# Kernel tuning notes

Hardware: AMD Instinct MI355X
Metric: run time of the kernel (lower is better)

The kernel has to match this reference:

```python
import jax, jax.numpy as jnp
import numpy as np

V, E, H = 32000, 512, 512
EH = 2 * H  # encoder output size (bidirectional)
B, T, S = 32, 64, 128


def setup_inputs() -> dict:
    key = jax.random.key(0)
    ks = jax.random.split(key, 16)
    s = 0.02
    return {
        "tgt_inputs": jax.random.randint(ks[0], (B, T), 0, V),
        "hidden": jax.random.normal(ks[1], (2, B, H), jnp.float32),
        "encoder_outputs": jax.random.normal(ks[2], (B, S, EH), jnp.float32),
        "src_mask": jnp.ones((B, S), jnp.bool_),
        "embedding": jax.random.normal(ks[3], (V, E), jnp.float32) * s,
        "Wa": jax.random.normal(ks[4], (EH, H), jnp.float32) * s,  # Linear(H -> 2H), weight [out,in]
        "w_ih0": jax.random.normal(ks[5], (3 * H, E + EH), jnp.float32) * s,
        "w_hh0": jax.random.normal(ks[6], (3 * H, H), jnp.float32) * s,
        "b_ih0": jax.random.normal(ks[7], (3 * H,), jnp.float32) * s,
        "b_hh0": jax.random.normal(ks[8], (3 * H,), jnp.float32) * s,
        "w_ih1": jax.random.normal(ks[9], (3 * H, H), jnp.float32) * s,
        "w_hh1": jax.random.normal(ks[10], (3 * H, H), jnp.float32) * s,
        "b_ih1": jax.random.normal(ks[11], (3 * H,), jnp.float32) * s,
        "b_hh1": jax.random.normal(ks[12], (3 * H,), jnp.float32) * s,
        "fc_w": jax.random.normal(ks[13], (V, H + EH), jnp.float32) * s,
        "fc_b": jax.random.normal(ks[14], (V,), jnp.float32) * s,
    }


def _gru_cell(x, h, w_ih, w_hh, b_ih, b_hh):
    # PyTorch GRU cell math
    gi = x @ w_ih.T + b_ih
    gh = h @ w_hh.T + b_hh
    i_r, i_z, i_n = jnp.split(gi, 3, axis=-1)
    h_r, h_z, h_n = jnp.split(gh, 3, axis=-1)
    r = jax.nn.sigmoid(i_r + h_r)
    z = jax.nn.sigmoid(i_z + h_z)
    n = jnp.tanh(i_n + r * h_n)
    return (1.0 - z) * n + z * h


def reference(tgt_inputs, hidden, encoder_outputs, src_mask, embedding, Wa,
              w_ih0, w_hh0, b_ih0, b_hh0, w_ih1, w_hh1, b_ih1, b_hh1,
              fc_w, fc_b):
    scale = 1.0 / jnp.sqrt(jnp.asarray(EH, encoder_outputs.dtype))

    def step(h, tok):
        emb = embedding[tok]                                   # [B,E]
        q = h[-1] @ Wa.T                                       # [B,2H] general attention
        scores = jnp.einsum('be,bse->bs', q, encoder_outputs) * scale
        scores = jnp.where(src_mask, scores, -jnp.inf)
        attn = jax.nn.softmax(scores, axis=-1)                 # [B,S]
        ctx = jnp.einsum('bs,bse->be', attn, encoder_outputs)  # [B,2H]
        x0 = jnp.concatenate([emb, ctx], axis=-1)              # [B,E+2H]
        h0 = _gru_cell(x0, h[0], w_ih0, w_hh0, b_ih0, b_hh0)
        h1 = _gru_cell(h0, h[1], w_ih1, w_hh1, b_ih1, b_hh1)
        logits = jnp.concatenate([h1, ctx], axis=-1) @ fc_w.T + fc_b  # [B,V]
        return jnp.stack([h0, h1]), logits

    # decode steps consume tokens 0..T-2 (teacher forcing)
    toks = tgt_inputs[:, :-1].T                                # [T-1,B]
    _, logits = jax.lax.scan(step, hidden, toks)
    return jnp.transpose(logits, (1, 0, 2))                    # [B,T-1,V]
```

## Files before the change

### kernel.cpp

```cpp
#include <hip/hip_runtime.h>
#include <cstdint>

typedef __attribute__((ext_vector_type(8))) short bf16x8;
typedef __attribute__((ext_vector_type(4))) float f32x4;
typedef __attribute__((ext_vector_type(2))) int i32x2;

__device__ __forceinline__ float bf2f(unsigned short u) {
  union { unsigned int i; float f; } v;
  v.i = ((unsigned int)u) << 16;
  return v.f;
}
__device__ __forceinline__ unsigned short f2bf(float f) {
  union { float f; unsigned int i; } v;
  v.f = f;
  unsigned int x = v.i;
  return (unsigned short)((x + 0x7FFFu + ((x >> 16) & 1u)) >> 16);
}

__device__ __forceinline__ void st_f32_coh(float* p, float v) {
  asm volatile("global_store_dword %0, %1, off sc0 sc1" :: "v"(p), "v"(v) : "memory");
}
__device__ __forceinline__ void st_u16_coh(unsigned short* p, unsigned int v) {
  asm volatile("global_store_short %0, %1, off sc0 sc1" :: "v"(p), "v"(v) : "memory");
}
__device__ __forceinline__ void st_b64_coh(void* p, i32x2 v) {
  asm volatile("global_store_dwordx2 %0, %1, off sc0 sc1" :: "v"(p), "v"(v) : "memory");
}

struct StepParams {
  const int* tgt;
  const int* mask;
  const float* embedding;
  const float* enc;
  const float* Wa;
  const float* hidden;
  const float* w_ih0; const float* w_hh0; const float* b_ih0; const float* b_hh0;
  const float* w_ih1; const float* w_hh1; const float* b_ih1; const float* b_hh1;
  float* h0buf;
  float* h1buf;
  float* x0b;
  unsigned short* encb;
  unsigned short* encwt;
  unsigned short* states;
  unsigned int* bars;
};

__device__ __forceinline__ void gbar(unsigned int* c) {
  asm volatile("s_waitcnt vmcnt(0)" ::: "memory");
  __syncthreads();
  if (threadIdx.x == 0) {
    __hip_atomic_fetch_add(c, 1u, __ATOMIC_RELAXED, __HIP_MEMORY_SCOPE_AGENT);
    while (__hip_atomic_load(c, __ATOMIC_RELAXED, __HIP_MEMORY_SCOPE_AGENT) < 256u)
      __builtin_amdgcn_s_sleep(1);
  }
  __syncthreads();
}

__device__ __forceinline__ void stage(const float* __restrict__ src, int ldk,
                                      int t0, int tid, float* __restrict__ xsh) {
#pragma unroll
  for (int u = 0; u < 32; u++)
    xsh[u * 257 + tid] = src[(size_t)u * ldk + t0 + tid];
}

__device__ __forceinline__ void gru_phase(
    const float* __restrict__ x, int xK,
    const float* __restrict__ hprev,
    const float* __restrict__ w_ih, const float* __restrict__ w_hh,
    const float* __restrict__ b_ih, const float* __restrict__ b_hh,
    float* __restrict__ hout, unsigned short* states, int srow,
    int w, int tid, float* xsh, float* red) {
  int b = tid & 31;
  int jl = (tid >> 5) & 1;
  int kq = tid >> 6;
  int j = w * 2 + jl;
  int kb = kq * 64;
  float gr = 0.f, gz = 0.f, gin = 0.f, ghn = 0.f;
  for (int t0 = 0; t0 < xK; t0 += 256) {
    __syncthreads();
    stage(x, xK, t0, tid, xsh);
    __syncthreads();
    const float4* w0p = (const float4*)(w_ih + (size_t)j * xK + t0 + kb);
    const float4* w1p = (const float4*)(w_ih + (size_t)(j + 512) * xK + t0 + kb);
    const float4* w2p = (const float4*)(w_ih + (size_t)(j + 1024) * xK + t0 + kb);
    const float* xr = xsh + b * 257 + kb;
#pragma unroll 4
    for (int k4 = 0; k4 < 16; k4++) {
      float4 wa = w0p[k4], wb = w1p[k4], wc = w2p[k4];
      float xv0 = xr[k4 * 4 + 0], xv1 = xr[k4 * 4 + 1];
      float xv2 = xr[k4 * 4 + 2], xv3 = xr[k4 * 4 + 3];
      gr = fmaf(wa.x, xv0, gr); gr = fmaf(wa.y, xv1, gr);
      gr = fmaf(wa.z, xv2, gr); gr = fmaf(wa.w, xv3, gr);
      gz = fmaf(wb.x, xv0, gz); gz = fmaf(wb.y, xv1, gz);
      gz = fmaf(wb.z, xv2, gz); gz = fmaf(wb.w, xv3, gz);
      gin = fmaf(wc.x, xv0, gin); gin = fmaf(wc.y, xv1, gin);
      gin = fmaf(wc.z, xv2, gin); gin = fmaf(wc.w, xv3, gin);
    }
  }
  for (int t0 = 0; t0 < 512; t0 += 256) {
    __syncthreads();
    stage(hprev, 512, t0, tid, xsh);
    __syncthreads();
    const float4* w0p = (const float4*)(w_hh + (size_t)j * 512 + t0 + kb);
    const float4* w1p = (const float4*)(w_hh + (size_t)(j + 512) * 512 + t0 + kb);
    const float4* w2p = (const float4*)(w_hh + (size_t)(j + 1024) * 512 + t0 + kb);
    const float* xr = xsh + b * 257 + kb;
#pragma unroll 4
    for (int k4 = 0; k4 < 16; k4++) {
      float4 wa = w0p[k4], wb = w1p[k4], wc = w2p[k4];
      float xv0 = xr[k4 * 4 + 0], xv1 = xr[k4 * 4 + 1];
      float xv2 = xr[k4 * 4 + 2], xv3 = xr[k4 * 4 + 3];
      gr = fmaf(wa.x, xv0, gr); gr = fmaf(wa.y, xv1, gr);
      gr = fmaf(wa.z, xv2, gr); gr = fmaf(wa.w, xv3, gr);
      gz = fmaf(wb.x, xv0, gz); gz = fmaf(wb.y, xv1, gz);
      gz = fmaf(wb.z, xv2, gz); gz = fmaf(wb.w, xv3, gz);
      ghn = fmaf(wc.x, xv0, ghn); ghn = fmaf(wc.y, xv1, ghn);
      ghn = fmaf(wc.z, xv2, ghn); ghn = fmaf(wc.w, xv3, ghn);
    }
  }
  red[tid * 4 + 0] = gr;
  red[tid * 4 + 1] = gz;
  red[tid * 4 + 2] = gin;
  red[tid * 4 + 3] = ghn;
  __syncthreads();
  if (tid < 64) {
#pragma unroll
    for (int g = 1; g < 4; g++) {
      gr += red[(tid + g * 64) * 4 + 0];
      gz += red[(tid + g * 64) * 4 + 1];
      gin += red[(tid + g * 64) * 4 + 2];
      ghn += red[(tid + g * 64) * 4 + 3];
    }
    gr += b_ih[j] + b_hh[j];
    gz += b_ih[j + 512] + b_hh[j + 512];
    gin += b_ih[j + 1024];
    ghn += b_hh[j + 1024];
    float r = 1.f / (1.f + __expf(-gr));
    float zz = 1.f / (1.f + __expf(-gz));
    float nv = gin + r * ghn;
    float e2 = __expf(-2.f * fabsf(nv));
    float th = (1.f - e2) / (1.f + e2);
    th = copysignf(th, nv);
    float hp = hprev[b * 512 + j];
    float hn = (1.f - zz) * th + zz * hp;
    st_f32_coh(hout + b * 512 + j, hn);
    if (states) states[(size_t)(srow + b) * 1536 + j] = f2bf(hn);
  }
}

__global__ __launch_bounds__(256, 1) void k_steps(StepParams p) {
  __shared__ float xsh[32 * 257];
  __shared__ float red[1024];
  __shared__ float h1sh[512];
  __shared__ float ssh[128];
  __shared__ float red2[128];
  int tid = threadIdx.x;
  int w = blockIdx.x;

  {
    int idx = w * 256 + tid;
    if (idx < 16384) st_f32_coh(p.h0buf + idx, p.hidden[idx]);
    else if (idx < 32768) st_f32_coh(p.h1buf + (idx - 16384), p.hidden[idx]);
    for (int r = 0; r < 16; r++) {
      size_t i4 = (size_t)r * 65536 + idx;
      float4 v = *(const float4*)(p.enc + i4 * 4);
      ushort4 o;
      o.x = f2bf(v.x); o.y = f2bf(v.y); o.z = f2bf(v.z); o.w = f2bf(v.w);
      union { ushort4 u; i32x2 d; } cv;
      cv.u = o;
      st_b64_coh(p.encb + i4 * 4, cv.d);
    }
    for (int blk = w; blk < 512; blk += 256) {
      int b = blk >> 4, s0 = (blk & 15) * 8;
      __syncthreads();
      for (int u = 0; u < 32; u++) {
        int f = u * 256 + tid;
        xsh[f] = p.enc[((size_t)b * 128 + s0 + (f >> 10)) * 1024 + (f & 1023)];
      }
      __syncthreads();
      float acc0[8] = {}, acc1[8] = {};
      for (int e = 0; e < 1024; e++) {
        float w0 = p.Wa[e * 512 + tid];
        float w1 = p.Wa[e * 512 + tid + 256];
#pragma unroll
        for (int si = 0; si < 8; si++) {
          float ev = xsh[si * 1024 + e];
          acc0[si] += w0 * ev;
          acc1[si] += w1 * ev;
        }
      }
#pragma unroll
      for (int si = 0; si < 8; si++) {
        st_u16_coh(p.encwt + ((size_t)b * 128 + s0 + si) * 512 + tid, f2bf(acc0[si]));
        st_u16_coh(p.encwt + ((size_t)b * 128 + s0 + si) * 512 + tid + 256, f2bf(acc1[si]));
      }
    }
  }
  unsigned int* bar = p.bars;
  gbar(bar++);

  int xcd = w & 7, loc = w >> 3;
  int ab = xcd * 4 + (loc >> 3);
  int ec = loc & 7;
  for (int t = 0; t < 63; t++) {
    const float* h1prev = p.h1buf + (size_t)t * 16384;
    float* x0t = p.x0b + (size_t)t * 49152;
    {
      float2 hv = *(const float2*)(h1prev + ab * 512 + tid * 2);
      h1sh[tid * 2] = hv.x;
      h1sh[tid * 2 + 1] = hv.y;
    }
    __syncthreads();
    {
      int s = tid & 127, part = tid >> 7;
      const unsigned short* ew = p.encwt + ((size_t)ab * 128 + s) * 512 + part * 256;
      const float* hh = h1sh + part * 256;
      float pacc = 0.f;
#pragma unroll 8
      for (int hc = 0; hc < 32; hc++) {
        bf16x8 v = *(const bf16x8*)(ew + hc * 8);
        const float* h8 = hh + hc * 8;
        pacc += bf2f((unsigned short)v[0]) * h8[0] + bf2f((unsigned short)v[1]) * h8[1]
              + bf2f((unsigned short)v[2]) * h8[2] + bf2f((unsigned short)v[3]) * h8[3]
              + bf2f((unsigned short)v[4]) * h8[4] + bf2f((unsigned short)v[5]) * h8[5]
              + bf2f((unsigned short)v[6]) * h8[6] + bf2f((unsigned short)v[7]) * h8[7];
      }
      red[tid] = pacc;
    }
    __syncthreads();
    if (tid < 128) {
      float sc = (red[tid] + red[tid + 128]) * 0.03125f;
      if (p.mask[ab * 128 + tid] == 0) sc = -__builtin_huge_valf();
      ssh[tid] = sc;
      red2[tid] = sc;
    }
    __syncthreads();
    for (int st = 64; st > 0; st >>= 1) {
      if (tid < st) red2[tid] = fmaxf(red2[tid], red2[tid + st]);
      __syncthreads();
    }
    float mx = red2[0];
    __syncthreads();
    if (tid < 128) {
      float e = __expf(ssh[tid] - mx);
      ssh[tid] = e;
      red2[tid] = e;
    }
    __syncthreads();
    for (int st = 64; st > 0; st >>= 1) {
      if (tid < st) red2[tid] += red2[tid + st];
      __syncthreads();
    }
    float inv = 1.f / red2[0];
    __syncthreads();
    if (tid < 128) ssh[tid] *= inv;
    __syncthreads();
    {
      int el = tid & 127, sh_ = tid >> 7;
      const unsigned short* eb = p.encb + (size_t)ab * 131072 + ec * 128 + el;
      int sbase = sh_ * 64;
      float c = 0.f;
#pragma unroll 8
      for (int s2 = 0; s2 < 64; s2++)
        c += ssh[sbase + s2] * bf2f(eb[(size_t)(sbase + s2) * 1024]);
      red[tid] = c;
    }
    __syncthreads();
    if (tid < 128) {
      float cv = red[tid] + red[tid + 128];
      st_f32_coh(x0t + ab * 1536 + 512 + ec * 128 + tid, cv);
      p.states[(size_t)(t * 32 + ab) * 1536 + 512 + ec * 128 + tid] = f2bf(cv);
    }
    {
      int tok = p.tgt[ab * 64 + t];
      if (tid < 64)
        st_f32_coh(x0t + ab * 1536 + ec * 64 + tid,
                   p.embedding[(size_t)tok * 512 + ec * 64 + tid]);
    }
    gbar(bar++);
    gru_phase(x0t, 1536, p.h0buf + (size_t)t * 16384, p.w_ih0, p.w_hh0, p.b_ih0,
              p.b_hh0, p.h0buf + (size_t)(t + 1) * 16384,
              (unsigned short*)nullptr, 0, w, tid, xsh, red);
    gbar(bar++);
    gru_phase(p.h0buf + (size_t)(t + 1) * 16384, 512, p.h1buf + (size_t)t * 16384,
              p.w_ih1, p.w_hh1, p.b_ih1, p.b_hh1,
              p.h1buf + (size_t)(t + 1) * 16384, p.states, t * 32, w, tid, xsh, red);
    gbar(bar++);
  }
}

__global__ __launch_bounds__(256) void k_cvt_fcw(const float* __restrict__ w,
                                                 unsigned short* __restrict__ o) {
  size_t i = ((size_t)blockIdx.x * 256 + threadIdx.x) * 8;
  float4 a = *(const float4*)(w + i);
  float4 b = *(const float4*)(w + i + 4);
  ushort4 lo, hi;
  lo.x = f2bf(a.x); lo.y = f2bf(a.y); lo.z = f2bf(a.z); lo.w = f2bf(a.w);
  hi.x = f2bf(b.x); hi.y = f2bf(b.y); hi.z = f2bf(b.z); hi.w = f2bf(b.w);
  *(ushort4*)(o + i) = lo;
  *(ushort4*)(o + i + 4) = hi;
}

template <bool PRE>
__global__ __launch_bounds__(256) void k_gemm(
    const unsigned short* __restrict__ states,
    const float* __restrict__ fc_w,
    const unsigned short* __restrict__ fcwb,
    const float* __restrict__ fc_b,
    float* __restrict__ out) {
  __shared__ unsigned short Ash[128 * 40];
  __shared__ unsigned short Bsh[128 * 40];
  int tid = threadIdx.x;
  int bx = blockIdx.x;
  int bid = (bx & 7) * 500 + (bx >> 3);
  int m0 = (bid & 15) * 128;
  int n0 = (bid >> 4) * 128;
  int lane = tid & 63, wave = tid >> 6;
  int q = lane >> 4, l16 = lane & 15;
  int wrow = (wave >> 1) * 64, wcol = (wave & 1) * 64;
  int arow = tid >> 1, ahalf = tid & 1;
  f32x4 acc[4][4] = {};
  const unsigned short* ag = states + (size_t)(m0 + arow) * 1536 + ahalf * 16;
  const float* bg = fc_w + (size_t)(n0 + arow) * 1536 + ahalf * 16;
  const unsigned short* bgb = PRE ? fcwb + (size_t)(n0 + arow) * 1536 + ahalf * 16 : nullptr;
  for (int k0 = 0; k0 < 1536; k0 += 32) {
    {
      const int4* src = (const int4*)(ag + k0);
      int4* dst = (int4*)(Ash + arow * 40 + ahalf * 16);
      dst[0] = src[0];
      dst[1] = src[1];
    }
    if constexpr (PRE) {
      const int4* src = (const int4*)(bgb + k0);
      int4* dst = (int4*)(Bsh + arow * 40 + ahalf * 16);
      dst[0] = src[0];
      dst[1] = src[1];
    } else {
      const float4* src = (const float4*)(bg + k0);
      __align__(16) unsigned short us[16];
#pragma unroll
      for (int i = 0; i < 4; i++) {
        float4 v = src[i];
        us[i * 4 + 0] = f2bf(v.x);
        us[i * 4 + 1] = f2bf(v.y);
        us[i * 4 + 2] = f2bf(v.z);
        us[i * 4 + 3] = f2bf(v.w);
      }
      int4* dst = (int4*)(Bsh + arow * 40 + ahalf * 16);
      dst[0] = ((int4*)us)[0];
      dst[1] = ((int4*)us)[1];
    }
    __syncthreads();
    bf16x8 av[4], bv[4];
#pragma unroll
    for (int i = 0; i < 4; i++) {
      av[i] = *(const bf16x8*)(Ash + (wrow + i * 16 + l16) * 40 + q * 8);
      bv[i] = *(const bf16x8*)(Bsh + (wcol + i * 16 + l16) * 40 + q * 8);
    }
#pragma unroll
    for (int mi = 0; mi < 4; mi++)
#pragma unroll
      for (int ni = 0; ni < 4; ni++)
        acc[mi][ni] = __builtin_amdgcn_mfma_f32_16x16x32_bf16(av[mi], bv[ni], acc[mi][ni], 0, 0, 0);
    __syncthreads();
  }
  float fb[4];
#pragma unroll
  for (int ni = 0; ni < 4; ni++) fb[ni] = fc_b[n0 + wcol + ni * 16 + l16];
#pragma unroll
  for (int mi = 0; mi < 4; mi++) {
#pragma unroll
    for (int r = 0; r < 4; r++) {
      int grow = m0 + wrow + mi * 16 + q * 4 + r;
      if (grow < 2016) {
        int tt = grow >> 5, bb = grow & 31;
        float* op = out + (size_t)bb * 2016000 + (size_t)tt * 32000 + n0 + wcol;
#pragma unroll
        for (int ni = 0; ni < 4; ni++)
          op[ni * 16 + l16] = acc[mi][ni][r] + fb[ni];
      }
    }
  }
}

extern "C" void kernel_launch(void* const* d_in, const int* in_sizes, int n_in,
                              void* d_out, int out_size, void* d_ws, size_t ws_size,
                              hipStream_t stream) {
  const int* tgt = (const int*)d_in[0];
  const float* hidden = (const float*)d_in[1];
  const float* enc = (const float*)d_in[2];
  const int* mask = (const int*)d_in[3];
  const float* embedding = (const float*)d_in[4];
  const float* Wa = (const float*)d_in[5];
  const float* w_ih0 = (const float*)d_in[6];
  const float* w_hh0 = (const float*)d_in[7];
  const float* b_ih0 = (const float*)d_in[8];
  const float* b_hh0 = (const float*)d_in[9];
  const float* w_ih1 = (const float*)d_in[10];
  const float* w_hh1 = (const float*)d_in[11];
  const float* b_ih1 = (const float*)d_in[12];
  const float* b_hh1 = (const float*)d_in[13];
  const float* fc_w = (const float*)d_in[14];
  const float* fc_b = (const float*)d_in[15];
  float* out = (float*)d_out;
  char* ws = (char*)d_ws;

  float* h0buf = (float*)(ws + 0);
  float* h1buf = (float*)(ws + 4194304);
  float* x0b = (float*)(ws + 8388608);
  unsigned short* encb = (unsigned short*)(ws + 20774912);
  unsigned short* encwt = (unsigned short*)(ws + 29163520);
  unsigned short* states = (unsigned short*)(ws + 33357824);
  unsigned int* bars = (unsigned int*)(ws + 39649280);
  const size_t FCWB_OFF = 41943040ull;
  unsigned short* fcwb = (unsigned short*)(ws + FCWB_OFF);
  bool pre = ws_size >= FCWB_OFF + 98304000ull;

  hipMemsetAsync(bars, 0, 4096, stream);
  if (pre) k_cvt_fcw<<<24000, 256, 0, stream>>>(fc_w, fcwb);

  StepParams p;
  p.tgt = tgt; p.mask = mask; p.embedding = embedding; p.enc = enc; p.Wa = Wa;
  p.hidden = hidden;
  p.w_ih0 = w_ih0; p.w_hh0 = w_hh0; p.b_ih0 = b_ih0; p.b_hh0 = b_hh0;
  p.w_ih1 = w_ih1; p.w_hh1 = w_hh1; p.b_ih1 = b_ih1; p.b_hh1 = b_hh1;
  p.h0buf = h0buf; p.h1buf = h1buf; p.x0b = x0b;
  p.encb = encb; p.encwt = encwt; p.states = states; p.bars = bars;

  k_steps<<<dim3(256), dim3(256), 0, stream>>>(p);

  if (pre) k_gemm<true><<<4000, 256, 0, stream>>>(states, fc_w, fcwb, fc_b, out);
  else k_gemm<false><<<4000, 256, 0, stream>>>(states, fc_w, nullptr, fc_b, out);
}
```

Baseline: 5.196 ms.

## Double threads per block in persistent decode kernel, splitting K reductions finer

Raises the persistent step kernel from 256 to 512 threads per block and re-partitions every phase (encoder preprocessing, attention scores, context, GRU matvecs) so each thread covers half the reduction range, with wider cross-thread reductions. The goal is more in-flight memory requests and latency hiding per CU in the latency-bound recurrent loop. The trade-off is extra shared-memory reduction work and larger __syncthreads costs. Some code paths may be inconsistent, for example the global barrier still counts 256 blocks and the GRU reduction now relies on red sized 2048.

```diff
diff --git a/kernel.cpp b/kernel.cpp
--- a/kernel.cpp
+++ b/kernel.cpp
@@ -56,13 +56,6 @@
   __syncthreads();
 }
 
-__device__ __forceinline__ void stage(const float* __restrict__ src, int ldk,
-                                      int t0, int tid, float* __restrict__ xsh) {
-#pragma unroll
-  for (int u = 0; u < 32; u++)
-    xsh[u * 257 + tid] = src[(size_t)u * ldk + t0 + tid];
-}
-
 __device__ __forceinline__ void gru_phase(
     const float* __restrict__ x, int xK,
     const float* __restrict__ hprev,
@@ -74,18 +67,23 @@
   int jl = (tid >> 5) & 1;
   int kq = tid >> 6;
   int j = w * 2 + jl;
-  int kb = kq * 64;
+  int kb = kq * 32;
   float gr = 0.f, gz = 0.f, gin = 0.f, ghn = 0.f;
   for (int t0 = 0; t0 < xK; t0 += 256) {
     __syncthreads();
-    stage(x, xK, t0, tid, xsh);
+#pragma unroll
+    for (int u = 0; u < 16; u++) {
+      int idx = u * 512 + tid;
+      xsh[(idx >> 8) * 257 + (idx & 255)] =
+          x[(size_t)(idx >> 8) * xK + t0 + (idx & 255)];
+    }
     __syncthreads();
     const float4* w0p = (const float4*)(w_ih + (size_t)j * xK + t0 + kb);
     const float4* w1p = (const float4*)(w_ih + (size_t)(j + 512) * xK + t0 + kb);
     const float4* w2p = (const float4*)(w_ih + (size_t)(j + 1024) * xK + t0 + kb);
     const float* xr = xsh + b * 257 + kb;
-#pragma unroll 4
-    for (int k4 = 0; k4 < 16; k4++) {
+#pragma unroll
+    for (int k4 = 0; k4 < 8; k4++) {
       float4 wa = w0p[k4], wb = w1p[k4], wc = w2p[k4];
       float xv0 = xr[k4 * 4 + 0], xv1 = xr[k4 * 4 + 1];
       float xv2 = xr[k4 * 4 + 2], xv3 = xr[k4 * 4 + 3];
@@ -99,14 +97,19 @@
   }
   for (int t0 = 0; t0 < 512; t0 += 256) {
     __syncthreads();
-    stage(hprev, 512, t0, tid, xsh);
+#pragma unroll
+    for (int u = 0; u < 16; u++) {
+      int idx = u * 512 + tid;
+      xsh[(idx >> 8) * 257 + (idx & 255)] =
+          hprev[(size_t)(idx >> 8) * 512 + t0 + (idx & 255)];
+    }
     __syncthreads();
     const float4* w0p = (const float4*)(w_hh + (size_t)j * 512 + t0 + kb);
     const float4* w1p = (const float4*)(w_hh + (size_t)(j + 512) * 512 + t0 + kb);
     const float4* w2p = (const float4*)(w_hh + (size_t)(j + 1024) * 512 + t0 + kb);
     const float* xr = xsh + b * 257 + kb;
-#pragma unroll 4
-    for (int k4 = 0; k4 < 16; k4++) {
+#pragma unroll
+    for (int k4 = 0; k4 < 8; k4++) {
       float4 wa = w0p[k4], wb = w1p[k4], wc = w2p[k4];
       float xv0 = xr[k4 * 4 + 0], xv1 = xr[k4 * 4 + 1];
       float xv2 = xr[k4 * 4 + 2], xv3 = xr[k4 * 4 + 3];
@@ -125,7 +128,7 @@
   __syncthreads();
   if (tid < 64) {
 #pragma unroll
-    for (int g = 1; g < 4; g++) {
+    for (int g = 1; g < 8; g++) {
       gr += red[(tid + g * 64) * 4 + 0];
       gz += red[(tid + g * 64) * 4 + 1];
       gin += red[(tid + g * 64) * 4 + 2];
@@ -148,9 +151,9 @@
   }
 }
 
-__global__ __launch_bounds__(256, 1) void k_steps(StepParams p) {
+__global__ __launch_bounds__(512, 4) void k_steps(StepParams p) {
   __shared__ float xsh[32 * 257];
-  __shared__ float red[1024];
+  __shared__ float red[2048];
   __shared__ float h1sh[512];
   __shared__ float ssh[128];
   __shared__ float red2[128];
@@ -158,11 +161,12 @@
   int w = blockIdx.x;
 
   {
-    int idx = w * 256 + tid;
+    int idx = w * 512 + tid;
     if (idx < 16384) st_f32_coh(p.h0buf + idx, p.hidden[idx]);
     else if (idx < 32768) st_f32_coh(p.h1buf + (idx - 16384), p.hidden[idx]);
-    for (int r = 0; r < 16; r++) {
-      size_t i4 = (size_t)r * 65536 + idx;
+#pragma unroll
+    for (int r = 0; r < 8; r++) {
+      size_t i4 = (size_t)r * 131072 + idx;
       float4 v = *(const float4*)(p.enc + i4 * 4);
       ushort4 o;
       o.x = f2bf(v.x); o.y = f2bf(v.y); o.z = f2bf(v.z); o.w = f2bf(v.w);
@@ -173,27 +177,21 @@
     for (int blk = w; blk < 512; blk += 256) {
       int b = blk >> 4, s0 = (blk & 15) * 8;
       __syncthreads();
-      for (int u = 0; u < 32; u++) {
-        int f = u * 256 + tid;
+#pragma unroll
+      for (int u = 0; u < 16; u++) {
+        int f = u * 512 + tid;
         xsh[f] = p.enc[((size_t)b * 128 + s0 + (f >> 10)) * 1024 + (f & 1023)];
       }
       __syncthreads();
-      float acc0[8] = {}, acc1[8] = {};
+      float acc[8] = {};
       for (int e = 0; e < 1024; e++) {
         float w0 = p.Wa[e * 512 + tid];
-        float w1 = p.Wa[e * 512 + tid + 256];
-#pragma unroll
-        for (int si = 0; si < 8; si++) {
-          float ev = xsh[si * 1024 + e];
-          acc0[si] += w0 * ev;
-          acc1[si] += w1 * ev;
-        }
+#pragma unroll
+        for (int si = 0; si < 8; si++) acc[si] += w0 * xsh[si * 1024 + e];
       }
 #pragma unroll
-      for (int si = 0; si < 8; si++) {
-        st_u16_coh(p.encwt + ((size_t)b * 128 + s0 + si) * 512 + tid, f2bf(acc0[si]));
-        st_u16_coh(p.encwt + ((size_t)b * 128 + s0 + si) * 512 + tid + 256, f2bf(acc1[si]));
-      }
+      for (int si = 0; si < 8; si++)
+        st_u16_coh(p.encwt + ((size_t)b * 128 + s0 + si) * 512 + tid, f2bf(acc[si]));
     }
   }
   unsigned int* bar = p.bars;
@@ -205,19 +203,15 @@
   for (int t = 0; t < 63; t++) {
     const float* h1prev = p.h1buf + (size_t)t * 16384;
     float* x0t = p.x0b + (size_t)t * 49152;
-    {
-      float2 hv = *(const float2*)(h1prev + ab * 512 + tid * 2);
-      h1sh[tid * 2] = hv.x;
-      h1sh[tid * 2 + 1] = hv.y;
-    }
+    h1sh[tid] = h1prev[ab * 512 + tid];
     __syncthreads();
     {
       int s = tid & 127, part = tid >> 7;
-      const unsigned short* ew = p.encwt + ((size_t)ab * 128 + s) * 512 + part * 256;
-      const float* hh = h1sh + part * 256;
+      const unsigned short* ew = p.encwt + ((size_t)ab * 128 + s) * 512 + part * 128;
+      const float* hh = h1sh + part * 128;
       float pacc = 0.f;
-#pragma unroll 8
-      for (int hc = 0; hc < 32; hc++) {
+#pragma unroll
+      for (int hc = 0; hc < 16; hc++) {
         bf16x8 v = *(const bf16x8*)(ew + hc * 8);
         const float* h8 = hh + hc * 8;
         pacc += bf2f((unsigned short)v[0]) * h8[0] + bf2f((unsigned short)v[1]) * h8[1]
@@ -229,7 +223,8 @@
     }
     __syncthreads();
     if (tid < 128) {
-      float sc = (red[tid] + red[tid + 128]) * 0.03125f;
+      float sc = red[tid] + red[tid + 128] + red[tid + 256] + red[tid + 384];
+      sc *= 0.03125f;
       if (p.mask[ab * 128 + tid] == 0) sc = -__builtin_huge_valf();
       ssh[tid] = sc;
       red2[tid] = sc;
@@ -258,16 +253,16 @@
     {
       int el = tid & 127, sh_ = tid >> 7;
       const unsigned short* eb = p.encb + (size_t)ab * 131072 + ec * 128 + el;
-      int sbase = sh_ * 64;
+      int sbase = sh_ * 32;
       float c = 0.f;
 #pragma unroll 8
-      for (int s2 = 0; s2 < 64; s2++)
+      for (int s2 = 0; s2 < 32; s2++)
         c += ssh[sbase + s2] * bf2f(eb[(size_t)(sbase + s2) * 1024]);
       red[tid] = c;
     }
     __syncthreads();
     if (tid < 128) {
-      float cv = red[tid] + red[tid + 128];
+      float cv = red[tid] + red[tid + 128] + red[tid + 256] + red[tid + 384];
       st_f32_coh(x0t + ab * 1536 + 512 + ec * 128 + tid, cv);
       p.states[(size_t)(t * 32 + ab) * 1536 + 512 + ec * 128 + tid] = f2bf(cv);
     }
@@ -427,7 +422,7 @@
   p.h0buf = h0buf; p.h1buf = h1buf; p.x0b = x0b;
   p.encb = encb; p.encwt = encwt; p.states = states; p.bars = bars;
 
-  k_steps<<<dim3(256), dim3(256), 0, stream>>>(p);
+  k_steps<<<dim3(256), dim3(512), 0, stream>>>(p);
 
   if (pre) k_gemm<true><<<4000, 256, 0, stream>>>(states, fc_w, fcwb, fc_b, out);
   else k_gemm<false><<<4000, 256, 0, stream>>>(states, fc_w, nullptr, fc_b, out);
```

After: 7.782 ms. 49.7% more time.
